# Kernel optimization log

Hardware: AMD Instinct MI355X
Metric: run time of the kernel (lower is better)

The kernel has to match this reference:

```python
import jax, jax.numpy as jnp
import numpy as np

L = 3000          # nodes per modality
M = 3             # modalities
N = L * M         # total nodes
E = 200000        # edges
D = 512           # hidden_dim
S = D // 4        # shared_dim = 128
EPS = 1e-12       # F.normalize eps


def _lrelu(x):
    return jax.nn.leaky_relu(x, negative_slope=0.01)


def _l2norm(x):
    n = jnp.linalg.norm(x, axis=-1, keepdims=True)
    return x / jnp.maximum(n, EPS)


def setup_inputs() -> dict:
    key = jax.random.key(0)
    ks = jax.random.split(key, 16)
    w = lambda k, shape: (jax.random.normal(k, shape, dtype=jnp.float32) * 0.02)
    inp = {
        "feat0": jax.random.normal(ks[0], (L, D), dtype=jnp.float32),
        "feat1": jax.random.normal(ks[1], (L, D), dtype=jnp.float32),
        "feat2": jax.random.normal(ks[2], (L, D), dtype=jnp.float32),
        "edge_index": jax.random.randint(ks[3], (2, E), 0, N, dtype=jnp.int64),
        # EdgeWeightGen params (torch Linear convention: weight is (out, in))
        "proj_w": w(ks[4], (S, D)),
        "mlp_w1": w(ks[5], (S, 2 * S)),
        "mlp_b1": jnp.zeros((S,), dtype=jnp.float32),
        "mlp_w2": w(ks[6], (1, S)),
        "mlp_b2": jnp.zeros((1,), dtype=jnp.float32),
        # CrossModalGraphLayer params, 2 layers
        "W1_0": w(ks[7], (D, D)),
        "W2_0": w(ks[8], (D, 2 * D)),
        "W1_1": w(ks[9], (D, D)),
        "W2_1": w(ks[10], (D, 2 * D)),
    }
    return inp


def reference(feat0, feat1, feat2, edge_index, proj_w, mlp_w1, mlp_b1,
              mlp_w2, mlp_b2, W1_0, W2_0, W1_1, W2_1):
    feature = jnp.concatenate([feat0, feat1, feat2], axis=0)  # (N, D)
    src, tgt = edge_index[0], edge_index[1]

    # EdgeWeightGen
    shared_src = _l2norm(feature[src] @ proj_w.T)   # (E, S)
    shared_tgt = _l2norm(feature[tgt] @ proj_w.T)   # (E, S)
    emb_cat = jnp.concatenate([shared_src, shared_tgt], axis=-1)  # (E, 2S)
    h = _lrelu(emb_cat @ mlp_w1.T + mlp_b1)
    edge_weight = jax.nn.sigmoid((h @ mlp_w2.T + mlp_b2)[:, 0])   # (E,)

    # build_adj_matrix: dense scatter-add (sparse_coo coalesce sums dups)
    adj = jnp.zeros((N, N), dtype=feature.dtype).at[src, tgt].add(edge_weight)
    row_sum = adj.sum(axis=1)
    d_inv_sqrt = jnp.where(row_sum > 0, row_sum ** -0.5, 0.0)
    # D^{-1/2} A D^{-1/2} as elementwise row/col scaling (same math as diag matmuls)
    gcn = d_inv_sqrt[:, None] * adj * d_inv_sqrt[None, :]

    # graph layers
    x = feature
    for W1, W2 in ((W1_0, W2_0), (W1_1, W2_1)):
        proj = x @ W1.T                 # (N, D)
        nb = gcn @ proj                 # (N, D)
        cat = jnp.concatenate([x + nb, x * nb], axis=-1)  # (N, 2D)
        x = _lrelu(cat @ W2.T)
    return x  # concatenated updated features; chunk(x, 3) recovers per-modal tuple
```

## Files before the change

kernel.cpp:

```cpp
#include <hip/hip_runtime.h>
#include <hip/hip_bf16.h>
#include <math.h>

#define NL 3000
#define NN 9000
#define NE 200000
#define DD 512
#define SS 128
#define MPAD 9088
#define MT   (MPAD/16)

typedef __attribute__((ext_vector_type(8))) short    bf16x8;
typedef __attribute__((ext_vector_type(8))) ushort   u16x8;
typedef __attribute__((ext_vector_type(4))) float    f32x4;

static __device__ __forceinline__ ushort f2bf(float f){
  unsigned u = __float_as_uint(f);
  return (ushort)((u + 0x7FFFu + ((u>>16)&1u)) >> 16);
}
static __device__ __forceinline__ float bf2f(ushort u){
  return __uint_as_float(((unsigned)u)<<16);
}

__global__ __launch_bounds__(256) void k_packall(const float* __restrict__ f0, const float* __restrict__ f1,
                        const float* __restrict__ f2, const float* __restrict__ pw,
                        const float* __restrict__ w1,
                        const float* __restrict__ W10, const float* __restrict__ W20,
                        const float* __restrict__ W11, const float* __restrict__ W21,
                        short* __restrict__ Ap1, short* __restrict__ BpF,
                        short* __restrict__ Bp10, short* __restrict__ Bp20,
                        short* __restrict__ Bp11, short* __restrict__ Bp21,
                        short* __restrict__ Bpab,
                        float* __restrict__ row_sum, int* __restrict__ cnt){
  int b = blockIdx.x;
  int lane = threadIdx.x & 63;
  if (b < 2272){
    int t = b*4 + (threadIdx.x>>6);
    int tm = t >> 4, tk = t & 15;
    int m = tm*16 + (lane&15);
    int k = tk*32 + (lane>>4)*8;
    float4 v0 = make_float4(0,0,0,0), v1 = v0;
    if (m < NN){
      const float* srow = (m < NL) ? f0 + (size_t)m*DD
                         : (m < 2*NL) ? f1 + (size_t)(m-NL)*DD
                         : f2 + (size_t)(m-2*NL)*DD;
      v0 = *(const float4*)(srow + k);
      v1 = *(const float4*)(srow + k + 4);
    }
    u16x8 r;
    r[0]=f2bf(v0.x); r[1]=f2bf(v0.y); r[2]=f2bf(v0.z); r[3]=f2bf(v0.w);
    r[4]=f2bf(v1.x); r[5]=f2bf(v1.y); r[6]=f2bf(v1.z); r[7]=f2bf(v1.w);
    *(u16x8*)(Ap1 + (size_t)t*512 + lane*8) = r;
  } else if (b < 3072){
    int t = (b-2272)*4 + (threadIdx.x>>6);
    const float* X; short* P; int K, ntk, lt;
    if (t < 128)      { X=pw;  P=BpF;  K=512;  ntk=16; lt=t; }
    else if (t < 640) { X=W10; P=Bp10; K=512;  ntk=16; lt=t-128; }
    else if (t < 1664){ X=W20; P=Bp20; K=1024; ntk=32; lt=t-640; }
    else if (t < 2176){ X=W11; P=Bp11; K=512;  ntk=16; lt=t-1664; }
    else              { X=W21; P=Bp21; K=1024; ntk=32; lt=t-2176; }
    int tm = lt/ntk, tk = lt - tm*ntk;
    int m = tm*16 + (lane&15);
    int k = tk*32 + (lane>>4)*8;
    float4 v0 = *(const float4*)(X + (size_t)m*K + k);
    float4 v1 = *(const float4*)(X + (size_t)m*K + k + 4);
    u16x8 r;
    r[0]=f2bf(v0.x); r[1]=f2bf(v0.y); r[2]=f2bf(v0.z); r[3]=f2bf(v0.w);
    r[4]=f2bf(v1.x); r[5]=f2bf(v1.y); r[6]=f2bf(v1.z); r[7]=f2bf(v1.w);
    *(u16x8*)(P + (size_t)lt*512 + lane*8) = r;
  } else if (b < 3088){
    int t = (b-3072)*4 + (threadIdx.x>>6);
    int tn = t >> 2, tk = t & 3;
    int n = tn*16 + (lane&15);
    int k = tk*32 + (lane>>4)*8;
    const float* sp = (n<128) ? (w1 + (size_t)n*256 + k) : (w1 + (size_t)(n-128)*256 + 128 + k);
    float4 v0 = *(const float4*)sp;
    float4 v1 = *(const float4*)(sp+4);
    u16x8 r;
    r[0]=f2bf(v0.x); r[1]=f2bf(v0.y); r[2]=f2bf(v0.z); r[3]=f2bf(v0.w);
    r[4]=f2bf(v1.x); r[5]=f2bf(v1.y); r[6]=f2bf(v1.z); r[7]=f2bf(v1.w);
    *(u16x8*)(Bpab + (size_t)t*512 + lane*8) = r;
  } else {
    int idx = (b-3088)*256 + threadIdx.x;
    for (int i=idx; i<NN; i+=4608){ row_sum[i]=0.f; cnt[i]=0; }
  }
}

template<int ACT, int OBF, int OPK>
__global__ __launch_bounds__(256) void k_gmm(const short* __restrict__ Ap, const short* __restrict__ Bp,
                                             void* __restrict__ Cv, short* __restrict__ Pk,
                                             int M, int N, int K){
  __shared__ short Bs[2048];
  int lane = threadIdx.x & 63, wave = threadIdx.x >> 6;
  int ktiles = K >> 5;
  int bm = blockIdx.y*128 + wave*32;
  int bn = blockIdx.x*64;
  const bf16x8* a0 = (const bf16x8*)(Ap + ((size_t)((bm>>4)  ) * ktiles)*512 + lane*8);
  const bf16x8* a1 = (const bf16x8*)(Ap + ((size_t)((bm>>4)+1) * ktiles)*512 + lane*8);
  const short*  bsrc = Bp + ((size_t)((bn>>4)+wave) * ktiles)*512 + lane*8;
  f32x4 acc[2][4];
  #pragma unroll
  for (int i=0;i<2;++i)
    #pragma unroll
    for (int j=0;j<4;++j) acc[i][j] = (f32x4){0.f,0.f,0.f,0.f};

  const bf16x8* bsh = (const bf16x8*)Bs;
  for (int kt=0; kt<ktiles; ++kt){
    u16x8 breg = *(const u16x8*)(bsrc + (size_t)kt*512);
    __syncthreads();
    *(u16x8*)&Bs[wave*512 + lane*8] = breg;
    __syncthreads();
    int off = kt*64;
    bf16x8 A0 = a0[off], A1 = a1[off];
    bf16x8 B0 = bsh[lane], B1 = bsh[64+lane], B2 = bsh[128+lane], B3 = bsh[192+lane];
    acc[0][0] = __builtin_amdgcn_mfma_f32_16x16x32_bf16(A0, B0, acc[0][0], 0,0,0);
    acc[0][1] = __builtin_amdgcn_mfma_f32_16x16x32_bf16(A0, B1, acc[0][1], 0,0,0);
    acc[0][2] = __builtin_amdgcn_mfma_f32_16x16x32_bf16(A0, B2, acc[0][2], 0,0,0);
    acc[0][3] = __builtin_amdgcn_mfma_f32_16x16x32_bf16(A0, B3, acc[0][3], 0,0,0);
    acc[1][0] = __builtin_amdgcn_mfma_f32_16x16x32_bf16(A1, B0, acc[1][0], 0,0,0);
    acc[1][1] = __builtin_amdgcn_mfma_f32_16x16x32_bf16(A1, B1, acc[1][1], 0,0,0);
    acc[1][2] = __builtin_amdgcn_mfma_f32_16x16x32_bf16(A1, B2, acc[1][2], 0,0,0);
    acc[1][3] = __builtin_amdgcn_mfma_f32_16x16x32_bf16(A1, B3, acc[1][3], 0,0,0);
  }
  int colo = lane & 15;
  int rowo = (lane >> 4) * 4;
  #pragma unroll
  for (int mi=0; mi<2; ++mi){
    #pragma unroll
    for (int r=0; r<4; ++r){
      int row = bm + mi*16 + rowo + r;
      if (row < M){
        #pragma unroll
        for (int ni=0; ni<4; ++ni){
          float v = acc[mi][ni][r];
          if (ACT) v = v>0.f ? v : 0.01f*v;
          int cidx = bn + ni*16 + colo;
          if (OBF) ((ushort*)Cv)[(size_t)row*N + cidx] = f2bf(v);
          else     ((float*) Cv)[(size_t)row*N + cidx] = v;
          if (OPK){
            size_t tl = (size_t)(row>>4)*16 + (cidx>>5);
            int pos = ((row&15) + ((cidx>>3)&3)*16)*8 + (cidx&7);
            Pk[tl*512 + pos] = (short)f2bf(v);
          }
        }
      }
    }
  }
}

__global__ __launch_bounds__(256) void k_l2n(const float* __restrict__ X, short* __restrict__ ShP){
  int lane = threadIdx.x & 63, wave = threadIdx.x >> 6;
  int m = blockIdx.x*4 + wave;
  float2 v = ((const float2*)(X + (size_t)m*SS))[lane];
  float ss = v.x*v.x + v.y*v.y;
  #pragma unroll
  for (int o=32;o>0;o>>=1) ss += __shfl_xor(ss, o);
  float inv = 1.f / fmaxf(sqrtf(ss), 1e-12f);
  int k = 2*lane;
  int tIdx = (m>>4)*4 + (k>>5);
  int pos  = ((m&15) + ((k>>3)&3)*16)*8 + (k&7);
  ushort2 r; r.x = f2bf(v.x*inv); r.y = f2bf(v.y*inv);
  *(ushort2*)(ShP + (size_t)tIdx*512 + pos) = r;
}

__global__ __launch_bounds__(256) void k_edge(const int* __restrict__ src, const int* __restrict__ tgt,
                      const ushort* __restrict__ AB,
                      const float* __restrict__ b1, const float* __restrict__ w2,
                      const float* __restrict__ b2p,
                      float* __restrict__ ew, float* __restrict__ row_sum, int* __restrict__ cnt){
  int lane = threadIdx.x & 63;
  int p = lane & 15, g = lane >> 4;
  int wid = blockIdx.x*(blockDim.x>>6) + (threadIdx.x>>6);
  int nw  = gridDim.x*(blockDim.x>>6);
  float4 b1a = ((const float4*)b1)[p*2], b1b = ((const float4*)b1)[p*2+1];
  float4 w2a = ((const float4*)w2)[p*2], w2b = ((const float4*)w2)[p*2+1];
  float bb[8] = {b1a.x,b1a.y,b1a.z,b1a.w,b1b.x,b1b.y,b1b.z,b1b.w};
  float ww[8] = {w2a.x,w2a.y,w2a.z,w2a.w,w2b.x,w2b.y,w2b.z,w2b.w};
  float b2 = b2p[0];
  for (int e = wid*4+g; e < NE; e += nw*4){
    int s = src[e], tg_ = tgt[e];
    u16x8 av = *(const u16x8*)(AB + (size_t)s*256 + p*8);
    u16x8 bv = *(const u16x8*)(AB + (size_t)tg_*256 + 128 + p*8);
    float acc = 0.f;
    #pragma unroll
    for (int i=0;i<8;++i){
      float h = bf2f(av[i]) + bf2f(bv[i]) + bb[i];
      h = h>0.f ? h : 0.01f*h;
      acc += h*ww[i];
    }
    acc += __shfl_xor(acc,1); acc += __shfl_xor(acc,2);
    acc += __shfl_xor(acc,4); acc += __shfl_xor(acc,8);
    if (p==0){
      float wgt = 1.f/(1.f+expf(-(acc+b2)));
      ew[e]=wgt;
      atomicAdd(&row_sum[s], wgt);
      atomicAdd(&cnt[s], 1);
    }
  }
}

__global__ __launch_bounds__(1024) void k_scan(const int* __restrict__ cnt, const float* __restrict__ row_sum,
                      int* __restrict__ row_ptr, float* __restrict__ dinv, int* __restrict__ fill){
  __shared__ int wsum[16];
  int t = threadIdx.x;
  int lane = t & 63, wid = t >> 6;
  const int CH = 9;
  int base = t*CH;
  int v[CH]; int s = 0;
  #pragma unroll
  for (int i=0;i<CH;++i){
    int idx = base+i;
    v[i] = (idx<NN) ? cnt[idx] : 0;
    s += v[i];
  }
  int ps = s;
  #pragma unroll
  for (int o=1;o<64;o<<=1){
    int x = __shfl_up(ps, o);
    if (lane >= o) ps += x;
  }
  if (lane==63) wsum[wid] = ps;
  __syncthreads();
  if (wid==0){
    int wv = (lane<16)? wsum[lane] : 0;
    #pragma unroll
    for (int o=1;o<16;o<<=1){
      int x = __shfl_up(wv, o);
      if (lane>=o) wv += x;
    }
    if (lane<16) wsum[lane]=wv;
  }
  __syncthreads();
  int prefix = (wid>0 ? wsum[wid-1] : 0) + (ps - s);
  #pragma unroll
  for (int i=0;i<CH;++i){
    int idx = base+i;
    if (idx<NN){
      row_ptr[idx] = prefix;
      float rs = row_sum[idx];
      dinv[idx] = rs>0.f ? (1.f/sqrtf(rs)) : 0.f;
      fill[idx] = 0;
      prefix += v[i];
    }
  }
  if (t==1023) row_ptr[NN] = wsum[15];
}

__global__ __launch_bounds__(256) void k_scatter(const int* __restrict__ src, const int* __restrict__ tgt,
                        const float* __restrict__ ew, const float* __restrict__ dinv,
                        const int* __restrict__ row_ptr, int* __restrict__ fill,
                        int* __restrict__ col, float* __restrict__ coef){
  int e = blockIdx.x*blockDim.x+threadIdx.x;
  if (e>=NE) return;
  int s=src[e], tg=tgt[e];
  int pos = atomicAdd(&fill[s],1);
  int idx = row_ptr[s]+pos;
  col[idx]=tg;
  coef[idx]=dinv[s]*ew[e]*dinv[tg];
}

template<int LAYER>
__global__ __launch_bounds__(128) void k_spmm_cat(const int* __restrict__ row_ptr, const int* __restrict__ col,
                     const float* __restrict__ coef, const ushort* __restrict__ proj,
                     const float* __restrict__ xf0, const float* __restrict__ xf1,
                     const float* __restrict__ xf2,
                     short* __restrict__ P){
  int m = blockIdx.x, t = threadIdx.x;
  int beg = row_ptr[m], end = row_ptr[m+1];
  float4 a0 = make_float4(0,0,0,0), a1 = a0, a2 = a0, a3 = a0;
  int j = beg;
  for (; j+4<=end; j+=4){
    int c0=col[j], c1=col[j+1], c2=col[j+2], c3=col[j+3];
    float w0=coef[j], w1=coef[j+1], w2_=coef[j+2], w3=coef[j+3];
    ushort4 p0 = ((const ushort4*)(proj + (size_t)c0*DD))[t];
    ushort4 p1 = ((const ushort4*)(proj + (size_t)c1*DD))[t];
    ushort4 p2 = ((const ushort4*)(proj + (size_t)c2*DD))[t];
    ushort4 p3 = ((const ushort4*)(proj + (size_t)c3*DD))[t];
    a0.x += w0*bf2f(p0.x); a0.y += w0*bf2f(p0.y); a0.z += w0*bf2f(p0.z); a0.w += w0*bf2f(p0.w);
    a1.x += w1*bf2f(p1.x); a1.y += w1*bf2f(p1.y); a1.z += w1*bf2f(p1.z); a1.w += w1*bf2f(p1.w);
    a2.x += w2_*bf2f(p2.x); a2.y += w2_*bf2f(p2.y); a2.z += w2_*bf2f(p2.z); a2.w += w2_*bf2f(p2.w);
    a3.x += w3*bf2f(p3.x); a3.y += w3*bf2f(p3.y); a3.z += w3*bf2f(p3.z); a3.w += w3*bf2f(p3.w);
  }
  for (; j<end; ++j){
    int c0=col[j]; float w0=coef[j];
    ushort4 p0 = ((const ushort4*)(proj + (size_t)c0*DD))[t];
    a0.x += w0*bf2f(p0.x); a0.y += w0*bf2f(p0.y); a0.z += w0*bf2f(p0.z); a0.w += w0*bf2f(p0.w);
  }
  a0.x += a1.x + a2.x + a3.x;
  a0.y += a1.y + a2.y + a3.y;
  a0.z += a1.z + a2.z + a3.z;
  a0.w += a1.w + a2.w + a3.w;
  const float* xrow;
  if (LAYER==0){
    xrow = (m < NL) ? xf0 + (size_t)m*DD
         : (m < 2*NL) ? xf1 + (size_t)(m-NL)*DD
         : xf2 + (size_t)(m-2*NL)*DD;
  } else {
    xrow = xf0 + (size_t)m*DD;
  }
  float4 xv = ((const float4*)xrow)[t];
  float ax = xv.x + a0.x, ay = xv.y + a0.y, az = xv.z + a0.z, aw = xv.w + a0.w;
  float mx = xv.x * a0.x, my = xv.y * a0.y, mz = xv.z * a0.z, mw = xv.w * a0.w;
  ushort4 ra, rm;
  ra.x=f2bf(ax); ra.y=f2bf(ay); ra.z=f2bf(az); ra.w=f2bf(aw);
  rm.x=f2bf(mx); rm.y=f2bf(my); rm.z=f2bf(mz); rm.w=f2bf(mw);
  size_t tileA = (size_t)((m>>4)*32 + (t>>3));
  int    off   = ((m&15) + ((t>>1)&3)*16)*8 + (t&1)*4;
  *(ushort4*)(P + tileA*512 + off)        = ra;
  *(ushort4*)(P + (tileA+16)*512 + off)   = rm;
}

extern "C" void kernel_launch(void* const* d_in, const int* in_sizes, int n_in,
                              void* d_out, int out_size, void* d_ws, size_t ws_size,
                              hipStream_t stream){
  const float* f0 = (const float*)d_in[0];
  const float* f1 = (const float*)d_in[1];
  const float* f2 = (const float*)d_in[2];
  const int*   ei = (const int*)d_in[3];
  const float* pw = (const float*)d_in[4];
  const float* w1 = (const float*)d_in[5];
  const float* b1 = (const float*)d_in[6];
  const float* w2 = (const float*)d_in[7];
  const float* b2 = (const float*)d_in[8];
  const float* W1_0 = (const float*)d_in[9];
  const float* W2_0 = (const float*)d_in[10];
  const float* W1_1 = (const float*)d_in[11];
  const float* W2_1 = (const float*)d_in[12];
  float* out = (float*)d_out;

  const int* src = ei;
  const int* tgt = ei + NE;

  char* base = (char*)d_ws;
  size_t o = 0;
  auto alloc = [&](size_t bytes)->char*{ char* p = base + o; o += (bytes + 1023) & ~size_t(1023); return p; };
  float* x1      = (float*)alloc((size_t)NN*DD*4);
  ushort* projbf = (ushort*)alloc((size_t)NN*DD*2);
  float* projS   = (float*)alloc((size_t)NN*SS*4);
  ushort* ABn    = (ushort*)alloc((size_t)NN*256*2);
  short* Apack1  = (short*)alloc((size_t)MT*16*1024);
  short* Apack2  = (short*)alloc((size_t)MT*32*1024);
  short* ShP     = (short*)alloc((size_t)MT*4*1024);
  short* BpF     = (short*)alloc((size_t)8*16*1024);
  short* Bpab    = (short*)alloc((size_t)16*4*1024);
  short* Bp10    = (short*)alloc((size_t)32*16*1024);
  short* Bp20    = (short*)alloc((size_t)32*32*1024);
  short* Bp11    = (short*)alloc((size_t)32*16*1024);
  short* Bp21    = (short*)alloc((size_t)32*32*1024);
  float* ew      = (float*)alloc(NE*4);
  float* coef    = (float*)alloc(NE*4);
  float* row_sum = (float*)alloc(NN*4);
  int*   cnt     = (int*)alloc(NN*4);
  float* dinv    = (float*)alloc(NN*4);
  int*   fill    = (int*)alloc(NN*4);
  int*   row_ptr = (int*)alloc((NN+1)*4);
  int*   col     = (int*)alloc(NE*4);

  k_packall<<<3106, 256, 0, stream>>>(f0,f1,f2,pw,w1,W1_0,W2_0,W1_1,W2_1,
                                      Apack1,BpF,Bp10,Bp20,Bp11,Bp21,Bpab,row_sum,cnt);

  dim3 gF(128/64, MPAD/128);
  k_gmm<0,0,0><<<gF, 256, 0, stream>>>(Apack1, BpF, projS, nullptr, NN, 128, 512);
  k_l2n<<<NN/4, 256, 0, stream>>>(projS, ShP);
  dim3 gAB(256/64, MPAD/128);
  k_gmm<0,1,0><<<gAB, 256, 0, stream>>>(ShP, Bpab, ABn, nullptr, NN, 256, 128);

  k_edge<<<2048, 256, 0, stream>>>(src,tgt,ABn,b1,w2,b2,ew,row_sum,cnt);
  k_scan<<<1, 1024, 0, stream>>>(cnt,row_sum,row_ptr,dinv,fill);
  k_scatter<<<(NE+255)/256, 256, 0, stream>>>(src,tgt,ew,dinv,row_ptr,fill,col,coef);

  dim3 gg(512/64, MPAD/128);
  k_gmm<0,1,0><<<gg, 256, 0, stream>>>(Apack1, Bp10, projbf, nullptr, NN, DD, DD);
  k_spmm_cat<0><<<NN, 128, 0, stream>>>(row_ptr, col, coef, projbf, f0, f1, f2, Apack2);
  k_gmm<1,0,1><<<gg, 256, 0, stream>>>(Apack2, Bp20, x1, Apack1, NN, DD, 2*DD);
  k_gmm<0,1,0><<<gg, 256, 0, stream>>>(Apack1, Bp11, projbf, nullptr, NN, DD, DD);
  k_spmm_cat<1><<<NN, 128, 0, stream>>>(row_ptr, col, coef, projbf, x1, nullptr, nullptr, Apack2);
  k_gmm<1,0,0><<<gg, 256, 0, stream>>>(Apack2, Bp21, out, nullptr, NN, DD, 2*DD);
}
```

Before: 360.2 us.

## Drop LDS staging in GEMM, remap block order, split fused output pack

The GEMM no longer stages B tiles through shared memory with two barriers per k-step. Each wave now loads all four B fragments directly from global memory, relying on cache for reuse. The launch grid becomes 1D with a swizzled block-to-tile mapping that groups 8 row tiles together, aimed at better L2 locality, and out-of-range blocks exit early. The scattered bf16 packed write in the layer-0 second GEMM epilogue is moved into a separate k_pack kernel, trading one extra launch and an extra read of x1 for a simpler epilogue.

```diff
diff --git a/kernel.cpp b/kernel.cpp
--- a/kernel.cpp
+++ b/kernel.cpp
@@ -86,33 +86,52 @@
   }
 }
 
-template<int ACT, int OBF, int OPK>
+__global__ __launch_bounds__(256) void k_pack(const float* __restrict__ X, short* __restrict__ P,
+                                              int M, int K, int nTilesK){
+  int t = blockIdx.x*4 + (threadIdx.x>>6);
+  int lane = threadIdx.x & 63;
+  int tm = t / nTilesK, tk = t - tm*nTilesK;
+  int m = tm*16 + (lane&15);
+  int k = tk*32 + (lane>>4)*8;
+  float4 v0 = make_float4(0,0,0,0), v1 = v0;
+  if (m < M){
+    v0 = *(const float4*)(X + (size_t)m*K + k);
+    v1 = *(const float4*)(X + (size_t)m*K + k + 4);
+  }
+  u16x8 r;
+  r[0]=f2bf(v0.x); r[1]=f2bf(v0.y); r[2]=f2bf(v0.z); r[3]=f2bf(v0.w);
+  r[4]=f2bf(v1.x); r[5]=f2bf(v1.y); r[6]=f2bf(v1.z); r[7]=f2bf(v1.w);
+  *(u16x8*)(P + (size_t)t*512 + lane*8) = r;
+}
+
+template<int ACT, int OBF>
 __global__ __launch_bounds__(256) void k_gmm(const short* __restrict__ Ap, const short* __restrict__ Bp,
-                                             void* __restrict__ Cv, short* __restrict__ Pk,
-                                             int M, int N, int K){
-  __shared__ short Bs[2048];
+                                             void* __restrict__ Cv, int M, int N, int K){
+  int l = blockIdx.x;
+  int rr = l & 7, tt = l >> 3;
+  int q = tt % 9, x = tt / 9;
+  int y = q*8 + rr;
+  if (y >= 71) return;
   int lane = threadIdx.x & 63, wave = threadIdx.x >> 6;
   int ktiles = K >> 5;
-  int bm = blockIdx.y*128 + wave*32;
-  int bn = blockIdx.x*64;
+  int bm = y*128 + wave*32;
+  int bn = x*64;
   const bf16x8* a0 = (const bf16x8*)(Ap + ((size_t)((bm>>4)  ) * ktiles)*512 + lane*8);
   const bf16x8* a1 = (const bf16x8*)(Ap + ((size_t)((bm>>4)+1) * ktiles)*512 + lane*8);
-  const short*  bsrc = Bp + ((size_t)((bn>>4)+wave) * ktiles)*512 + lane*8;
+  const bf16x8* b0 = (const bf16x8*)(Bp + ((size_t)((bn>>4)  ) * ktiles)*512 + lane*8);
+  const bf16x8* b1 = (const bf16x8*)(Bp + ((size_t)((bn>>4)+1) * ktiles)*512 + lane*8);
+  const bf16x8* b2 = (const bf16x8*)(Bp + ((size_t)((bn>>4)+2) * ktiles)*512 + lane*8);
+  const bf16x8* b3 = (const bf16x8*)(Bp + ((size_t)((bn>>4)+3) * ktiles)*512 + lane*8);
   f32x4 acc[2][4];
   #pragma unroll
   for (int i=0;i<2;++i)
     #pragma unroll
     for (int j=0;j<4;++j) acc[i][j] = (f32x4){0.f,0.f,0.f,0.f};
 
-  const bf16x8* bsh = (const bf16x8*)Bs;
   for (int kt=0; kt<ktiles; ++kt){
-    u16x8 breg = *(const u16x8*)(bsrc + (size_t)kt*512);
-    __syncthreads();
-    *(u16x8*)&Bs[wave*512 + lane*8] = breg;
-    __syncthreads();
     int off = kt*64;
     bf16x8 A0 = a0[off], A1 = a1[off];
-    bf16x8 B0 = bsh[lane], B1 = bsh[64+lane], B2 = bsh[128+lane], B3 = bsh[192+lane];
+    bf16x8 B0 = b0[off], B1 = b1[off], B2 = b2[off], B3 = b3[off];
     acc[0][0] = __builtin_amdgcn_mfma_f32_16x16x32_bf16(A0, B0, acc[0][0], 0,0,0);
     acc[0][1] = __builtin_amdgcn_mfma_f32_16x16x32_bf16(A0, B1, acc[0][1], 0,0,0);
     acc[0][2] = __builtin_amdgcn_mfma_f32_16x16x32_bf16(A0, B2, acc[0][2], 0,0,0);
@@ -137,11 +156,6 @@
           int cidx = bn + ni*16 + colo;
           if (OBF) ((ushort*)Cv)[(size_t)row*N + cidx] = f2bf(v);
           else     ((float*) Cv)[(size_t)row*N + cidx] = v;
-          if (OPK){
-            size_t tl = (size_t)(row>>4)*16 + (cidx>>5);
-            int pos = ((row&15) + ((cidx>>3)&3)*16)*8 + (cidx&7);
-            Pk[tl*512 + pos] = (short)f2bf(v);
-          }
         }
       }
     }
@@ -359,21 +373,19 @@
   k_packall<<<3106, 256, 0, stream>>>(f0,f1,f2,pw,w1,W1_0,W2_0,W1_1,W2_1,
                                       Apack1,BpF,Bp10,Bp20,Bp11,Bp21,Bpab,row_sum,cnt);
 
-  dim3 gF(128/64, MPAD/128);
-  k_gmm<0,0,0><<<gF, 256, 0, stream>>>(Apack1, BpF, projS, nullptr, NN, 128, 512);
+  k_gmm<0,0><<<2*72, 256, 0, stream>>>(Apack1, BpF, projS, NN, 128, 512);
   k_l2n<<<NN/4, 256, 0, stream>>>(projS, ShP);
-  dim3 gAB(256/64, MPAD/128);
-  k_gmm<0,1,0><<<gAB, 256, 0, stream>>>(ShP, Bpab, ABn, nullptr, NN, 256, 128);
+  k_gmm<0,1><<<4*72, 256, 0, stream>>>(ShP, Bpab, ABn, NN, 256, 128);
 
   k_edge<<<2048, 256, 0, stream>>>(src,tgt,ABn,b1,w2,b2,ew,row_sum,cnt);
   k_scan<<<1, 1024, 0, stream>>>(cnt,row_sum,row_ptr,dinv,fill);
   k_scatter<<<(NE+255)/256, 256, 0, stream>>>(src,tgt,ew,dinv,row_ptr,fill,col,coef);
 
-  dim3 gg(512/64, MPAD/128);
-  k_gmm<0,1,0><<<gg, 256, 0, stream>>>(Apack1, Bp10, projbf, nullptr, NN, DD, DD);
+  k_gmm<0,1><<<8*72, 256, 0, stream>>>(Apack1, Bp10, projbf, NN, DD, DD);
   k_spmm_cat<0><<<NN, 128, 0, stream>>>(row_ptr, col, coef, projbf, f0, f1, f2, Apack2);
-  k_gmm<1,0,1><<<gg, 256, 0, stream>>>(Apack2, Bp20, x1, Apack1, NN, DD, 2*DD);
-  k_gmm<0,1,0><<<gg, 256, 0, stream>>>(Apack1, Bp11, projbf, nullptr, NN, DD, DD);
+  k_gmm<1,0><<<8*72, 256, 0, stream>>>(Apack2, Bp20, x1, NN, DD, 2*DD);
+  k_pack<<<MT*16/4, 256, 0, stream>>>(x1, Apack1, NN, DD, 16);
+  k_gmm<0,1><<<8*72, 256, 0, stream>>>(Apack1, Bp11, projbf, NN, DD, DD);
   k_spmm_cat<1><<<NN, 128, 0, stream>>>(row_ptr, col, coef, projbf, x1, nullptr, nullptr, Apack2);
-  k_gmm<1,0,0><<<gg, 256, 0, stream>>>(Apack2, Bp21, out, nullptr, NN, DD, 2*DD);
-}
+  k_gmm<1,0><<<8*72, 256, 0, stream>>>(Apack2, Bp21, out, NN, DD, 2*DD);
+}
```

Result: faster. 322.6 us (-10.4%).
